# Optimization experiments

Measured on AMD Instinct MI355X. Metric: run time of the kernel, lower is better.

## Reference

```python
import jax, jax.numpy as jnp
import numpy as np

N, F, E, G = 100000, 128, 600000, 1000
EPS = 1e-5


def setup_inputs() -> dict:
    key = jax.random.key(0)
    k1, k2, k3, k4 = jax.random.split(key, 4)
    x = jax.random.normal(k1, (N, F), dtype=jnp.float32)
    graph_id = jnp.sort(jax.random.randint(k2, (N,), 0, G, dtype=jnp.int32))
    edge_src = jax.random.randint(k3, (E,), 0, N, dtype=jnp.int32)
    edge_dst = jax.random.randint(k4, (E,), 0, N, dtype=jnp.int32)
    return {
        "x": x,
        "gamma": jnp.ones((F,), jnp.float32),
        "beta": jnp.zeros((F,), jnp.float32),
        "lambda_batch": jnp.ones((F,), jnp.float32),
        "lambda_graph": jnp.ones((F,), jnp.float32),
        "lambda_adja": jnp.ones((F,), jnp.float32),
        "lambda_node": jnp.ones((F,), jnp.float32),
        "graph_id": graph_id,
        "edge_src": edge_src,
        "edge_dst": edge_dst,
    }


def _batch_norm(x):
    # BatchNorm1d in training mode: biased stats over the node (batch) axis.
    mu = jnp.mean(x, axis=0, keepdims=True)
    var = jnp.mean(jnp.square(x), axis=0, keepdims=True) - jnp.square(mu)
    return (x - mu) * jax.lax.rsqrt(var + EPS)


def _graph_norm(x, graph_id):
    # Per-graph mean/var per feature via segment reductions. graph_id: [N]
    ones = jnp.ones((x.shape[0],), x.dtype)
    cnt = jax.ops.segment_sum(ones, graph_id, num_segments=G)  # [G]
    cnt = jnp.maximum(cnt, 1.0)[:, None]
    s = jax.ops.segment_sum(x, graph_id, num_segments=G)               # [G,F]
    s2 = jax.ops.segment_sum(jnp.square(x), graph_id, num_segments=G)  # [G,F]
    mu = s / cnt
    var = jnp.maximum(s2 / cnt - jnp.square(mu), 0.0)
    return (x - mu[graph_id]) * jax.lax.rsqrt(var[graph_id] + EPS)


def _adja_node_norm(x, edge_src, edge_dst):
    # Per-node stats over in-neighbors: normalize x_i with mean/var of {x_j : j->i}.
    msg = x[edge_src]  # [E,F]
    deg = jax.ops.segment_sum(jnp.ones((E,), x.dtype), edge_dst, num_segments=N)
    deg = jnp.maximum(deg, 1.0)[:, None]
    s = jax.ops.segment_sum(msg, edge_dst, num_segments=N)
    s2 = jax.ops.segment_sum(jnp.square(msg), edge_dst, num_segments=N)
    mu = s / deg
    var = jnp.maximum(s2 / deg - jnp.square(mu), 0.0)
    return (x - mu) * jax.lax.rsqrt(var + EPS)


def _node_norm(x):
    # LayerNorm over feature axis, no affine.
    mu = jnp.mean(x, axis=-1, keepdims=True)
    var = jnp.mean(jnp.square(x - mu), axis=-1, keepdims=True)
    return (x - mu) * jax.lax.rsqrt(var + EPS)


def reference(x, gamma, beta, lambda_batch, lambda_graph, lambda_adja,
              lambda_node, graph_id, edge_src, edge_dst):
    x_b = _batch_norm(x)
    x_g = _graph_norm(x, graph_id)
    x_a = _adja_node_norm(x, edge_src, edge_dst)
    x_n = _node_norm(x)
    # norm_lambda(): softmax across the four lambda vectors per feature.
    lam = jax.nn.softmax(jnp.stack([lambda_batch, lambda_graph, lambda_adja,
                                    lambda_node], axis=0), axis=0)  # [4,F]
    x_new = lam[0] * x_b + lam[1] * x_g + lam[2] * x_a + lam[3] * x_n
    return gamma * x_new + beta
```

## Files before the change

kernel.cpp:

```cpp
#include <hip/hip_runtime.h>

#define N_NODES 100000
#define NF      128
#define NE      600000
#define NG      1000
#define EPSF    1e-5f

#define STATS_NB (N_NODES / 32)
#define DEG_NB   (((NE / 4) + 255) / 256)
#define ALLOC_NB ((N_NODES + 255) / 256)
#define BRED_NB  64
#define PREP_NB  ((NG * NF) / 256 + 1)

__global__ __launch_bounds__(256) void k1_stats_deg(
    const float* __restrict__ x, const int* __restrict__ gid,
    const int* __restrict__ edst,
    float* __restrict__ gsum, float* __restrict__ gsq, int* __restrict__ cnt,
    int* __restrict__ deg)
{
    if (blockIdx.x >= STATS_NB) {
        int t = (blockIdx.x - STATS_NB) * 256 + threadIdx.x;
        if (t < NE / 4) {
            const int4 d4 = reinterpret_cast<const int4*>(edst)[t];
            atomicAdd(&deg[d4.x], 1);
            atomicAdd(&deg[d4.y], 1);
            atomicAdd(&deg[d4.z], 1);
            atomicAdd(&deg[d4.w], 1);
        }
        return;
    }
    const int wave = threadIdx.x >> 6;
    const int lane = threadIdx.x & 63;
    const int f = lane * 2;
    const int r0 = blockIdx.x * 32 + wave * 8;
    const int r1 = r0 + 8;

    float gsx = 0.f, gsy = 0.f, gqx = 0.f, gqy = 0.f;
    int cur = gid[r0];
    int runStart = r0;

    for (int r = r0; r < r1; ++r) {
        int g = gid[r];
        if (g != cur) {
            atomicAdd(&gsum[cur * NF + f],     gsx);
            atomicAdd(&gsum[cur * NF + f + 1], gsy);
            atomicAdd(&gsq [cur * NF + f],     gqx);
            atomicAdd(&gsq [cur * NF + f + 1], gqy);
            if (lane == 0) atomicAdd(&cnt[cur], r - runStart);
            gsx = gsy = gqx = gqy = 0.f;
            cur = g; runStart = r;
        }
        const float2 v = *reinterpret_cast<const float2*>(x + (size_t)r * NF + f);
        gsx += v.x; gsy += v.y; gqx += v.x * v.x; gqy += v.y * v.y;
    }
    atomicAdd(&gsum[cur * NF + f],     gsx);
    atomicAdd(&gsum[cur * NF + f + 1], gsy);
    atomicAdd(&gsq [cur * NF + f],     gqx);
    atomicAdd(&gsq [cur * NF + f + 1], gqy);
    if (lane == 0) atomicAdd(&cnt[cur], r1 - runStart);
}

__global__ __launch_bounds__(256) void k2_alloc_bred(
    const int* __restrict__ deg, int2* __restrict__ odeg, int* __restrict__ cursor,
    int* __restrict__ total,
    const float* __restrict__ gsum, const float* __restrict__ gsq,
    float* __restrict__ bsum, float* __restrict__ bsq)
{
    if (blockIdx.x < ALLOC_NB) {
        const int i = blockIdx.x * 256 + threadIdx.x;
        const int lane = threadIdx.x & 63;
        int d = (i < N_NODES) ? deg[i] : 0;
        int p = d;
#pragma unroll
        for (int st = 1; st < 64; st <<= 1) {
            int v = __shfl_up(p, st, 64);
            if (lane >= st) p += v;
        }
        int wtot = __shfl(p, 63, 64);
        int base = 0;
        if (lane == 63) base = atomicAdd(total, wtot);
        base = __shfl(base, 63, 64);
        if (i < N_NODES) {
            int o = base + p - d;
            odeg[i] = make_int2(o, d);
            cursor[i] = o;
        }
    } else {
        int b = blockIdx.x - ALLOC_NB;
        int t = threadIdx.x;
        int f = t & 127, gl = t >> 7;
        float s = 0.f, q = 0.f;
#pragma unroll
        for (int k = 0; k < 8; ++k) {
            int g = b * 16 + gl * 8 + k;
            if (g < NG) { s += gsum[g * NF + f]; q += gsq[g * NF + f]; }
        }
        atomicAdd(&bsum[f], s);
        atomicAdd(&bsq[f], q);
    }
}

__global__ __launch_bounds__(256) void k3_fill_prep(
    const int* __restrict__ esrc, const int* __restrict__ edst,
    int* __restrict__ cursor, int* __restrict__ nbr,
    float* __restrict__ gsum, float* __restrict__ gsq, const int* __restrict__ cnt,
    const float* __restrict__ bsum, const float* __restrict__ bsq,
    const float* __restrict__ gamma, const float* __restrict__ beta,
    const float* __restrict__ lb, const float* __restrict__ lg,
    const float* __restrict__ la, const float* __restrict__ ln,
    float* __restrict__ fc)
{
    if (blockIdx.x < DEG_NB) {
        int t = blockIdx.x * 256 + threadIdx.x;
        if (t < NE / 4) {
            const int4 d4 = reinterpret_cast<const int4*>(edst)[t];
            const int4 s4 = reinterpret_cast<const int4*>(esrc)[t];
            int p;
            p = atomicAdd(&cursor[d4.x], 1); nbr[p] = s4.x;
            p = atomicAdd(&cursor[d4.y], 1); nbr[p] = s4.y;
            p = atomicAdd(&cursor[d4.z], 1); nbr[p] = s4.z;
            p = atomicAdd(&cursor[d4.w], 1); nbr[p] = s4.w;
        }
        return;
    }
    int b = blockIdx.x - DEG_NB;
    if (b < (NG * NF) / 256) {
        int idx = b * 256 + threadIdx.x;
        int g = idx >> 7;
        float c = (float)cnt[g]; if (c < 1.f) c = 1.f;
        float rc = 1.0f / c;
        float m = gsum[idx] * rc;
        float v = gsq[idx] * rc - m * m; if (v < 0.f) v = 0.f;
        gsum[idx] = m;
        gsq[idx]  = rsqrtf(v + EPSF);
    } else if (threadIdx.x < NF) {
        int f = threadIdx.x;
        float mb = bsum[f] * (1.0f / N_NODES);
        float vb = bsq[f] * (1.0f / N_NODES) - mb * mb;
        float rvb = rsqrtf(vb + EPSF);
        float l0 = lb[f], l1 = lg[f], l2 = la[f], l3 = ln[f];
        float m = fmaxf(fmaxf(l0, l1), fmaxf(l2, l3));
        float w0 = __expf(l0 - m), w1 = __expf(l1 - m), w2 = __expf(l2 - m), w3 = __expf(l3 - m);
        float rs = gamma[f] / (w0 + w1 + w2 + w3);
        float* p = fc + f * 8;
        p[0] = mb; p[1] = rvb;
        p[2] = w0 * rs; p[3] = w1 * rs; p[4] = w2 * rs; p[5] = w3 * rs;
        p[6] = beta[f]; p[7] = 0.f;
    }
}

__global__ __launch_bounds__(256) void k5_final(
    const float* __restrict__ x, const int* __restrict__ gid,
    const float* __restrict__ gmu, const float* __restrict__ grs,
    const float* __restrict__ fc, const int2* __restrict__ odeg,
    const int* __restrict__ nbr, float* __restrict__ out)
{
    const int wave = threadIdx.x >> 6;
    const int lane = threadIdx.x & 63;
    const int i0 = blockIdx.x * 8 + wave * 2;
    const int i1 = i0 + 1;
    const int f = lane * 2;

    const float2 xa = *reinterpret_cast<const float2*>(x + (size_t)i0 * NF + f);
    const float2 xb = *reinterpret_cast<const float2*>(x + (size_t)i1 * NF + f);

    const float4 c0 = *reinterpret_cast<const float4*>(fc + f * 8);
    const float4 c1 = *reinterpret_cast<const float4*>(fc + f * 8 + 4);
    const float4 d0 = *reinterpret_cast<const float4*>(fc + (f + 1) * 8);
    const float4 d1 = *reinterpret_cast<const float4*>(fc + (f + 1) * 8 + 4);

    const int2 oa = odeg[i0], ob = odeg[i1];
    const int sa = oa.x, da = oa.y, sb = ob.x, db = ob.y;
    float asx = 0.f, asy = 0.f, aqx = 0.f, aqy = 0.f;
    float bsx = 0.f, bsy = 0.f, bqx = 0.f, bqy = 0.f;
    int ka = 0, kb = 0;
    while (ka < da || kb < db) {
        int ia_[8], ib_[8];
        const bool hA = ka < da, hB = kb < db;
        if (hA) {
#pragma unroll
            for (int k = 0; k < 8; ++k)
                ia_[k] = nbr[(ka + k < da) ? (sa + ka + k) : sa];
        }
        if (hB) {
#pragma unroll
            for (int k = 0; k < 8; ++k)
                ib_[k] = nbr[(kb + k < db) ? (sb + kb + k) : sb];
        }
        if (hA) {
#pragma unroll
            for (int k = 0; k < 8; ++k) {
                const float2 v = *reinterpret_cast<const float2*>(x + (size_t)ia_[k] * NF + f);
                const float m = (ka + k < da) ? 1.f : 0.f;
                asx += m * v.x; asy += m * v.y;
                aqx += m * v.x * v.x; aqy += m * v.y * v.y;
            }
        }
        if (hB) {
#pragma unroll
            for (int k = 0; k < 8; ++k) {
                const float2 v = *reinterpret_cast<const float2*>(x + (size_t)ib_[k] * NF + f);
                const float m = (kb + k < db) ? 1.f : 0.f;
                bsx += m * v.x; bsy += m * v.y;
                bqx += m * v.x * v.x; bqy += m * v.y * v.y;
            }
        }
        ka += 8; kb += 8;
    }

    float xba_x = (xa.x - c0.x) * c0.y, xba_y = (xa.y - d0.x) * d0.y;
    float xbb_x = (xb.x - c0.x) * c0.y, xbb_y = (xb.y - d0.x) * d0.y;

    const int ga = gid[i0], gb = gid[i1];
    const float2 mga = *reinterpret_cast<const float2*>(gmu + (size_t)ga * NF + f);
    const float2 rga = *reinterpret_cast<const float2*>(grs + (size_t)ga * NF + f);
    const float2 mgb = *reinterpret_cast<const float2*>(gmu + (size_t)gb * NF + f);
    const float2 rgb = *reinterpret_cast<const float2*>(grs + (size_t)gb * NF + f);
    float xga_x = (xa.x - mga.x) * rga.x, xga_y = (xa.y - mga.y) * rga.y;
    float xgb_x = (xb.x - mgb.x) * rgb.x, xgb_y = (xb.y - mgb.y) * rgb.y;

    float sA = xa.x + xa.y, sB = xb.x + xb.y;
#pragma unroll
    for (int d = 1; d < 64; d <<= 1) { sA += __shfl_xor(sA, d, 64); sB += __shfl_xor(sB, d, 64); }
    const float mnA = sA * (1.0f / NF), mnB = sB * (1.0f / NF);
    float dax = xa.x - mnA, day = xa.y - mnA, dbx = xb.x - mnB, dby = xb.y - mnB;
    float qA = dax * dax + day * day, qB = dbx * dbx + dby * dby;
#pragma unroll
    for (int d = 1; d < 64; d <<= 1) { qA += __shfl_xor(qA, d, 64); qB += __shfl_xor(qB, d, 64); }
    const float rvnA = rsqrtf(qA * (1.0f / NF) + EPSF);
    const float rvnB = rsqrtf(qB * (1.0f / NF) + EPSF);
    float xna_x = dax * rvnA, xna_y = day * rvnA;
    float xnb_x = dbx * rvnB, xnb_y = dby * rvnB;

    float dga = (float)da; if (dga < 1.f) dga = 1.f;
    float dgb = (float)db; if (dgb < 1.f) dgb = 1.f;
    float rda = 1.0f / dga, rdb = 1.0f / dgb;
    float maa = asx * rda, mab = asy * rda;
    float vaa = aqx * rda - maa * maa; if (vaa < 0.f) vaa = 0.f;
    float vab = aqy * rda - mab * mab; if (vab < 0.f) vab = 0.f;
    float xaa_x = (xa.x - maa) * rsqrtf(vaa + EPSF);
    float xaa_y = (xa.y - mab) * rsqrtf(vab + EPSF);
    float mba = bsx * rdb, mbb = bsy * rdb;
    float vba = bqx * rdb - mba * mba; if (vba < 0.f) vba = 0.f;
    float vbb = bqy * rdb - mbb * mbb; if (vbb < 0.f) vbb = 0.f;
    float xab_x = (xb.x - mba) * rsqrtf(vba + EPSF);
    float xab_y = (xb.y - mbb) * rsqrtf(vbb + EPSF);

    float oa_x = c0.z * xba_x + c0.w * xga_x + c1.x * xaa_x + c1.y * xna_x + c1.z;
    float oa_y = d0.z * xba_y + d0.w * xga_y + d1.x * xaa_y + d1.y * xna_y + d1.z;
    float ob_x = c0.z * xbb_x + c0.w * xgb_x + c1.x * xab_x + c1.y * xnb_x + c1.z;
    float ob_y = d0.z * xbb_y + d0.w * xgb_y + d1.x * xab_y + d1.y * xnb_y + d1.z;
    *reinterpret_cast<float2*>(out + (size_t)i0 * NF + f) = make_float2(oa_x, oa_y);
    *reinterpret_cast<float2*>(out + (size_t)i1 * NF + f) = make_float2(ob_x, ob_y);
}

extern "C" void kernel_launch(void* const* d_in, const int* in_sizes, int n_in,
                              void* d_out, int out_size, void* d_ws, size_t ws_size,
                              hipStream_t stream) {
    const float* x     = (const float*)d_in[0];
    const float* gamma = (const float*)d_in[1];
    const float* beta  = (const float*)d_in[2];
    const float* lb    = (const float*)d_in[3];
    const float* lg    = (const float*)d_in[4];
    const float* la    = (const float*)d_in[5];
    const float* ln    = (const float*)d_in[6];
    const int*   gid   = (const int*)d_in[7];
    const int*   esrc  = (const int*)d_in[8];
    const int*   edst  = (const int*)d_in[9];
    float*       out   = (float*)d_out;

    float* ws    = (float*)d_ws;
    float* bsum  = ws;
    float* bsq   = bsum + NF;
    float* gsum  = bsq + NF;
    float* gsq   = gsum + (size_t)NG * NF;
    int*   cnt   = (int*)(gsq + (size_t)NG * NF);
    int*   deg   = cnt + NG;
    int*   total = deg + N_NODES;
    int*   cursor= total + 2;
    int2*  odeg  = (int2*)(cursor + N_NODES);
    int*   nbr   = (int*)(odeg + N_NODES);
    float* fc    = (float*)(nbr + NE);

    const size_t zero_elems = (size_t)2 * NF + (size_t)2 * NG * NF + NG + N_NODES + 2;
    hipMemsetAsync(d_ws, 0, zero_elems * sizeof(float), stream);

    k1_stats_deg<<<STATS_NB + DEG_NB, 256, 0, stream>>>(
        x, gid, edst, gsum, gsq, cnt, deg);
    k2_alloc_bred<<<ALLOC_NB + BRED_NB, 256, 0, stream>>>(
        deg, odeg, cursor, total, gsum, gsq, bsum, bsq);
    k3_fill_prep<<<DEG_NB + PREP_NB, 256, 0, stream>>>(
        esrc, edst, cursor, nbr, gsum, gsq, cnt, bsum, bsq,
        gamma, beta, lb, lg, la, ln, fc);
    k5_final<<<N_NODES / 8, 256, 0, stream>>>(
        x, gid, gsum, gsq, fc, odeg, nbr, out);
}
```

Before: 288.5 us.

## Fold stats finalization into final kernel and process one node per wave

Moves the per-graph mean/rsqrt, batch-norm stats and lambda softmax computation out of the fill kernel and recomputes them inline in the final kernel from raw sums. The final kernel now handles one node per wave instead of two interleaved nodes, doubling the grid, and writes output with nontemporal stores. This drops the prep blocks and the fc buffer, at the cost of redundant per-thread softmax/rsqrt work and less per-wave memory-level parallelism in the neighbor gather.

```diff
diff --git a/kernel.cpp b/kernel.cpp
--- a/kernel.cpp
+++ b/kernel.cpp
@@ -10,7 +10,8 @@
 #define DEG_NB   (((NE / 4) + 255) / 256)
 #define ALLOC_NB ((N_NODES + 255) / 256)
 #define BRED_NB  64
-#define PREP_NB  ((NG * NF) / 256 + 1)
+
+typedef float v2f __attribute__((ext_vector_type(2)));
 
 __global__ __launch_bounds__(256) void k1_stats_deg(
     const float* __restrict__ x, const int* __restrict__ gid,
@@ -100,158 +101,113 @@
     }
 }
 
-__global__ __launch_bounds__(256) void k3_fill_prep(
+__global__ __launch_bounds__(256) void k3_fill(
     const int* __restrict__ esrc, const int* __restrict__ edst,
-    int* __restrict__ cursor, int* __restrict__ nbr,
-    float* __restrict__ gsum, float* __restrict__ gsq, const int* __restrict__ cnt,
+    int* __restrict__ cursor, int* __restrict__ nbr)
+{
+    int t = blockIdx.x * 256 + threadIdx.x;
+    if (t < NE / 4) {
+        const int4 d4 = reinterpret_cast<const int4*>(edst)[t];
+        const int4 s4 = reinterpret_cast<const int4*>(esrc)[t];
+        int p;
+        p = atomicAdd(&cursor[d4.x], 1); nbr[p] = s4.x;
+        p = atomicAdd(&cursor[d4.y], 1); nbr[p] = s4.y;
+        p = atomicAdd(&cursor[d4.z], 1); nbr[p] = s4.z;
+        p = atomicAdd(&cursor[d4.w], 1); nbr[p] = s4.w;
+    }
+}
+
+__global__ __launch_bounds__(256) void k5_final(
+    const float* __restrict__ x, const int* __restrict__ gid,
+    const float* __restrict__ gsum, const float* __restrict__ gsq,
+    const int* __restrict__ cnt,
     const float* __restrict__ bsum, const float* __restrict__ bsq,
     const float* __restrict__ gamma, const float* __restrict__ beta,
     const float* __restrict__ lb, const float* __restrict__ lg,
     const float* __restrict__ la, const float* __restrict__ ln,
-    float* __restrict__ fc)
-{
-    if (blockIdx.x < DEG_NB) {
-        int t = blockIdx.x * 256 + threadIdx.x;
-        if (t < NE / 4) {
-            const int4 d4 = reinterpret_cast<const int4*>(edst)[t];
-            const int4 s4 = reinterpret_cast<const int4*>(esrc)[t];
-            int p;
-            p = atomicAdd(&cursor[d4.x], 1); nbr[p] = s4.x;
-            p = atomicAdd(&cursor[d4.y], 1); nbr[p] = s4.y;
-            p = atomicAdd(&cursor[d4.z], 1); nbr[p] = s4.z;
-            p = atomicAdd(&cursor[d4.w], 1); nbr[p] = s4.w;
-        }
-        return;
-    }
-    int b = blockIdx.x - DEG_NB;
-    if (b < (NG * NF) / 256) {
-        int idx = b * 256 + threadIdx.x;
-        int g = idx >> 7;
-        float c = (float)cnt[g]; if (c < 1.f) c = 1.f;
-        float rc = 1.0f / c;
-        float m = gsum[idx] * rc;
-        float v = gsq[idx] * rc - m * m; if (v < 0.f) v = 0.f;
-        gsum[idx] = m;
-        gsq[idx]  = rsqrtf(v + EPSF);
-    } else if (threadIdx.x < NF) {
-        int f = threadIdx.x;
-        float mb = bsum[f] * (1.0f / N_NODES);
-        float vb = bsq[f] * (1.0f / N_NODES) - mb * mb;
-        float rvb = rsqrtf(vb + EPSF);
-        float l0 = lb[f], l1 = lg[f], l2 = la[f], l3 = ln[f];
-        float m = fmaxf(fmaxf(l0, l1), fmaxf(l2, l3));
-        float w0 = __expf(l0 - m), w1 = __expf(l1 - m), w2 = __expf(l2 - m), w3 = __expf(l3 - m);
-        float rs = gamma[f] / (w0 + w1 + w2 + w3);
-        float* p = fc + f * 8;
-        p[0] = mb; p[1] = rvb;
-        p[2] = w0 * rs; p[3] = w1 * rs; p[4] = w2 * rs; p[5] = w3 * rs;
-        p[6] = beta[f]; p[7] = 0.f;
-    }
-}
-
-__global__ __launch_bounds__(256) void k5_final(
-    const float* __restrict__ x, const int* __restrict__ gid,
-    const float* __restrict__ gmu, const float* __restrict__ grs,
-    const float* __restrict__ fc, const int2* __restrict__ odeg,
-    const int* __restrict__ nbr, float* __restrict__ out)
+    const int2* __restrict__ odeg, const int* __restrict__ nbr,
+    float* __restrict__ out)
 {
     const int wave = threadIdx.x >> 6;
     const int lane = threadIdx.x & 63;
-    const int i0 = blockIdx.x * 8 + wave * 2;
-    const int i1 = i0 + 1;
+    const int i = blockIdx.x * 4 + wave;
     const int f = lane * 2;
-
-    const float2 xa = *reinterpret_cast<const float2*>(x + (size_t)i0 * NF + f);
-    const float2 xb = *reinterpret_cast<const float2*>(x + (size_t)i1 * NF + f);
-
-    const float4 c0 = *reinterpret_cast<const float4*>(fc + f * 8);
-    const float4 c1 = *reinterpret_cast<const float4*>(fc + f * 8 + 4);
-    const float4 d0 = *reinterpret_cast<const float4*>(fc + (f + 1) * 8);
-    const float4 d1 = *reinterpret_cast<const float4*>(fc + (f + 1) * 8 + 4);
-
-    const int2 oa = odeg[i0], ob = odeg[i1];
-    const int sa = oa.x, da = oa.y, sb = ob.x, db = ob.y;
+    const int f1 = f + 1;
+
+    const float2 xi = *reinterpret_cast<const float2*>(x + (size_t)i * NF + f);
+
+    const int2 od = odeg[i];
+    const int s0 = od.x, dg = od.y;
     float asx = 0.f, asy = 0.f, aqx = 0.f, aqy = 0.f;
-    float bsx = 0.f, bsy = 0.f, bqx = 0.f, bqy = 0.f;
-    int ka = 0, kb = 0;
-    while (ka < da || kb < db) {
-        int ia_[8], ib_[8];
-        const bool hA = ka < da, hB = kb < db;
-        if (hA) {
-#pragma unroll
-            for (int k = 0; k < 8; ++k)
-                ia_[k] = nbr[(ka + k < da) ? (sa + ka + k) : sa];
-        }
-        if (hB) {
-#pragma unroll
-            for (int k = 0; k < 8; ++k)
-                ib_[k] = nbr[(kb + k < db) ? (sb + kb + k) : sb];
-        }
-        if (hA) {
-#pragma unroll
-            for (int k = 0; k < 8; ++k) {
-                const float2 v = *reinterpret_cast<const float2*>(x + (size_t)ia_[k] * NF + f);
-                const float m = (ka + k < da) ? 1.f : 0.f;
-                asx += m * v.x; asy += m * v.y;
-                aqx += m * v.x * v.x; aqy += m * v.y * v.y;
-            }
-        }
-        if (hB) {
-#pragma unroll
-            for (int k = 0; k < 8; ++k) {
-                const float2 v = *reinterpret_cast<const float2*>(x + (size_t)ib_[k] * NF + f);
-                const float m = (kb + k < db) ? 1.f : 0.f;
-                bsx += m * v.x; bsy += m * v.y;
-                bqx += m * v.x * v.x; bqy += m * v.y * v.y;
-            }
-        }
-        ka += 8; kb += 8;
-    }
-
-    float xba_x = (xa.x - c0.x) * c0.y, xba_y = (xa.y - d0.x) * d0.y;
-    float xbb_x = (xb.x - c0.x) * c0.y, xbb_y = (xb.y - d0.x) * d0.y;
-
-    const int ga = gid[i0], gb = gid[i1];
-    const float2 mga = *reinterpret_cast<const float2*>(gmu + (size_t)ga * NF + f);
-    const float2 rga = *reinterpret_cast<const float2*>(grs + (size_t)ga * NF + f);
-    const float2 mgb = *reinterpret_cast<const float2*>(gmu + (size_t)gb * NF + f);
-    const float2 rgb = *reinterpret_cast<const float2*>(grs + (size_t)gb * NF + f);
-    float xga_x = (xa.x - mga.x) * rga.x, xga_y = (xa.y - mga.y) * rga.y;
-    float xgb_x = (xb.x - mgb.x) * rgb.x, xgb_y = (xb.y - mgb.y) * rgb.y;
-
-    float sA = xa.x + xa.y, sB = xb.x + xb.y;
-#pragma unroll
-    for (int d = 1; d < 64; d <<= 1) { sA += __shfl_xor(sA, d, 64); sB += __shfl_xor(sB, d, 64); }
-    const float mnA = sA * (1.0f / NF), mnB = sB * (1.0f / NF);
-    float dax = xa.x - mnA, day = xa.y - mnA, dbx = xb.x - mnB, dby = xb.y - mnB;
-    float qA = dax * dax + day * day, qB = dbx * dbx + dby * dby;
-#pragma unroll
-    for (int d = 1; d < 64; d <<= 1) { qA += __shfl_xor(qA, d, 64); qB += __shfl_xor(qB, d, 64); }
-    const float rvnA = rsqrtf(qA * (1.0f / NF) + EPSF);
-    const float rvnB = rsqrtf(qB * (1.0f / NF) + EPSF);
-    float xna_x = dax * rvnA, xna_y = day * rvnA;
-    float xnb_x = dbx * rvnB, xnb_y = dby * rvnB;
-
-    float dga = (float)da; if (dga < 1.f) dga = 1.f;
-    float dgb = (float)db; if (dgb < 1.f) dgb = 1.f;
-    float rda = 1.0f / dga, rdb = 1.0f / dgb;
-    float maa = asx * rda, mab = asy * rda;
-    float vaa = aqx * rda - maa * maa; if (vaa < 0.f) vaa = 0.f;
-    float vab = aqy * rda - mab * mab; if (vab < 0.f) vab = 0.f;
-    float xaa_x = (xa.x - maa) * rsqrtf(vaa + EPSF);
-    float xaa_y = (xa.y - mab) * rsqrtf(vab + EPSF);
-    float mba = bsx * rdb, mbb = bsy * rdb;
-    float vba = bqx * rdb - mba * mba; if (vba < 0.f) vba = 0.f;
-    float vbb = bqy * rdb - mbb * mbb; if (vbb < 0.f) vbb = 0.f;
-    float xab_x = (xb.x - mba) * rsqrtf(vba + EPSF);
-    float xab_y = (xb.y - mbb) * rsqrtf(vbb + EPSF);
-
-    float oa_x = c0.z * xba_x + c0.w * xga_x + c1.x * xaa_x + c1.y * xna_x + c1.z;
-    float oa_y = d0.z * xba_y + d0.w * xga_y + d1.x * xaa_y + d1.y * xna_y + d1.z;
-    float ob_x = c0.z * xbb_x + c0.w * xgb_x + c1.x * xab_x + c1.y * xnb_x + c1.z;
-    float ob_y = d0.z * xbb_y + d0.w * xgb_y + d1.x * xab_y + d1.y * xnb_y + d1.z;
-    *reinterpret_cast<float2*>(out + (size_t)i0 * NF + f) = make_float2(oa_x, oa_y);
-    *reinterpret_cast<float2*>(out + (size_t)i1 * NF + f) = make_float2(ob_x, ob_y);
+    for (int e = 0; e < dg; e += 8) {
+        int idx[8];
+#pragma unroll
+        for (int k = 0; k < 8; ++k)
+            idx[k] = nbr[(e + k < dg) ? (s0 + e + k) : s0];
+#pragma unroll
+        for (int k = 0; k < 8; ++k) {
+            const float2 v = *reinterpret_cast<const float2*>(x + (size_t)idx[k] * NF + f);
+            const float m = (e + k < dg) ? 1.f : 0.f;
+            asx += m * v.x; asy += m * v.y;
+            aqx += m * v.x * v.x; aqy += m * v.y * v.y;
+        }
+    }
+
+    const float invN = 1.0f / (float)N_NODES;
+    float mbx = bsum[f]  * invN, mby = bsum[f1] * invN;
+    float vbx = bsq[f]  * invN - mbx * mbx;
+    float vby = bsq[f1] * invN - mby * mby;
+    float rvbx = rsqrtf(vbx + EPSF), rvby = rsqrtf(vby + EPSF);
+
+    float l0x = lb[f],  l1x = lg[f],  l2x = la[f],  l3x = ln[f];
+    float l0y = lb[f1], l1y = lg[f1], l2y = la[f1], l3y = ln[f1];
+    float mx = fmaxf(fmaxf(l0x, l1x), fmaxf(l2x, l3x));
+    float my = fmaxf(fmaxf(l0y, l1y), fmaxf(l2y, l3y));
+    float w0x = __expf(l0x - mx), w1x = __expf(l1x - mx), w2x = __expf(l2x - mx), w3x = __expf(l3x - mx);
+    float w0y = __expf(l0y - my), w1y = __expf(l1y - my), w2y = __expf(l2y - my), w3y = __expf(l3y - my);
+    float rsx = gamma[f]  / (w0x + w1x + w2x + w3x);
+    float rsy = gamma[f1] / (w0y + w1y + w2y + w3y);
+    w0x *= rsx; w1x *= rsx; w2x *= rsx; w3x *= rsx;
+    w0y *= rsy; w1y *= rsy; w2y *= rsy; w3y *= rsy;
+    const float btx = beta[f], bty = beta[f1];
+
+    float xbx = (xi.x - mbx) * rvbx;
+    float xby = (xi.y - mby) * rvby;
+
+    const int g = gid[i];
+    float c = (float)cnt[g]; if (c < 1.f) c = 1.f;
+    float rc = 1.0f / c;
+    const float2 gs = *reinterpret_cast<const float2*>(gsum + (size_t)g * NF + f);
+    const float2 gq = *reinterpret_cast<const float2*>(gsq  + (size_t)g * NF + f);
+    float mgx = gs.x * rc, mgy = gs.y * rc;
+    float vgx = gq.x * rc - mgx * mgx; if (vgx < 0.f) vgx = 0.f;
+    float vgy = gq.y * rc - mgy * mgy; if (vgy < 0.f) vgy = 0.f;
+    float xgx = (xi.x - mgx) * rsqrtf(vgx + EPSF);
+    float xgy = (xi.y - mgy) * rsqrtf(vgy + EPSF);
+
+    float s = xi.x + xi.y;
+#pragma unroll
+    for (int d = 1; d < 64; d <<= 1) s += __shfl_xor(s, d, 64);
+    const float mn = s * (1.0f / NF);
+    float dxx = xi.x - mn, dyy = xi.y - mn;
+    float q = dxx * dxx + dyy * dyy;
+#pragma unroll
+    for (int d = 1; d < 64; d <<= 1) q += __shfl_xor(q, d, 64);
+    const float rvn = rsqrtf(q * (1.0f / NF) + EPSF);
+    float xnx = dxx * rvn, xny = dyy * rvn;
+
+    float dgc = (float)dg; if (dgc < 1.f) dgc = 1.f;
+    float rdg = 1.0f / dgc;
+    float max_ = asx * rdg, may_ = asy * rdg;
+    float vax = aqx * rdg - max_ * max_; if (vax < 0.f) vax = 0.f;
+    float vay = aqy * rdg - may_ * may_; if (vay < 0.f) vay = 0.f;
+    float xax = (xi.x - max_) * rsqrtf(vax + EPSF);
+    float xay = (xi.y - may_) * rsqrtf(vay + EPSF);
+
+    v2f o;
+    o.x = w0x * xbx + w1x * xgx + w2x * xax + w3x * xnx + btx;
+    o.y = w0y * xby + w1y * xgy + w2y * xay + w3y * xny + bty;
+    __builtin_nontemporal_store(o, reinterpret_cast<v2f*>(out + (size_t)i * NF + f));
 }
 
 extern "C" void kernel_launch(void* const* d_in, const int* in_sizes, int n_in,
@@ -280,7 +236,6 @@
     int*   cursor= total + 2;
     int2*  odeg  = (int2*)(cursor + N_NODES);
     int*   nbr   = (int*)(odeg + N_NODES);
-    float* fc    = (float*)(nbr + NE);
 
     const size_t zero_elems = (size_t)2 * NF + (size_t)2 * NG * NF + NG + N_NODES + 2;
     hipMemsetAsync(d_ws, 0, zero_elems * sizeof(float), stream);
@@ -289,9 +244,8 @@
         x, gid, edst, gsum, gsq, cnt, deg);
     k2_alloc_bred<<<ALLOC_NB + BRED_NB, 256, 0, stream>>>(
         deg, odeg, cursor, total, gsum, gsq, bsum, bsq);
-    k3_fill_prep<<<DEG_NB + PREP_NB, 256, 0, stream>>>(
-        esrc, edst, cursor, nbr, gsum, gsq, cnt, bsum, bsq,
-        gamma, beta, lb, lg, la, ln, fc);
-    k5_final<<<N_NODES / 8, 256, 0, stream>>>(
-        x, gid, gsum, gsq, fc, odeg, nbr, out);
-}
+    k3_fill<<<DEG_NB, 256, 0, stream>>>(esrc, edst, cursor, nbr);
+    k5_final<<<N_NODES / 4, 256, 0, stream>>>(
+        x, gid, gsum, gsq, cnt, bsum, bsq, gamma, beta, lb, lg, la, ln,
+        odeg, nbr, out);
+}
```

Measured after the change: 290.8 us. Within noise of the previous version (+0.8%).
